# Optimization experiments

Hardware: AMD Instinct MI355X
Metric: run time of the kernel (lower is better)

The kernel has to match this reference:

```python
import jax, jax.numpy as jnp
import numpy as np

DIM = 4096
NUM_EXPERTS = 64
TOP_K = 8
TOKENS = 16384

def setup_inputs() -> dict:
    key = jax.random.key(0)
    kx, kw = jax.random.split(key)
    x = jax.random.normal(kx, (TOKENS, DIM), dtype=jnp.float32)
    # gate weight as in nn.Linear(dim, num_experts, bias=False): shape [num_experts, dim]
    W = jax.random.normal(kw, (NUM_EXPERTS, DIM), dtype=jnp.float32) * 0.02
    return {"x": x, "W": W}

def reference(x, W):
    # logits = x @ W^T : [tokens, num_experts]
    logits = jnp.einsum('td,ed->te', x, W)
    top_k_values, top_k_indices = jax.lax.top_k(logits, TOP_K)
    # softmax over top-k values in float32, cast back to x dtype
    scores = jax.nn.softmax(top_k_values.astype(jnp.float32), axis=-1).astype(x.dtype)
    return scores, top_k_indices
```

## Files before the change

### kernel.cpp

```cpp
#include <hip/hip_runtime.h>
#include <math.h>

typedef float  f32x4 __attribute__((ext_vector_type(4)));
typedef short  s16x8 __attribute__((ext_vector_type(8)));
typedef unsigned short u16x8 __attribute__((ext_vector_type(8)));
typedef unsigned int   u32x4 __attribute__((ext_vector_type(4)));

constexpr int TOKENS  = 16384;
constexpr int DIM     = 4096;
constexpr int NE      = 64;
constexpr int TOPK    = 8;
constexpr int KB      = 32;
constexpr int NIT     = DIM / KB;
constexpr int WAVES   = 8;
constexpr int KSL     = DIM / WAVES;
constexpr int NITW    = KSL / KB;
constexpr int LISTCAP = 16384;
constexpr float GAPTH = 1e-4f;

constexpr unsigned WARR_U16   = (unsigned)NIT * 4 * 64 * 8;
constexpr size_t   WS_INT_OFF = (size_t)WARR_U16 * 2 * sizeof(unsigned short);
constexpr size_t   WS_NEEDED  = WS_INT_OFF + sizeof(int) * (size_t)(16 + LISTCAP);

__device__ __forceinline__ unsigned short bf_rne(float f) {
    unsigned u = __float_as_uint(f);
    u += 0x7FFFu + ((u >> 16) & 1u);
    return (unsigned short)(u >> 16);
}
__device__ __forceinline__ float bf_f32(unsigned short h) {
    return __uint_as_float(((unsigned)h) << 16);
}
__device__ __forceinline__ uint2 cvt_pair(float f0, float f1) {
    unsigned short h0 = bf_rne(f0);
    unsigned short h1 = bf_rne(f1);
    uint2 r;
    r.x = (unsigned)h0 | ((unsigned)h1 << 16);
    r.y = (unsigned)bf_rne(f0 - bf_f32(h0)) | ((unsigned)bf_rne(f1 - bf_f32(h1)) << 16);
    return r;
}
union Cvt { u32x4 u; s16x8 s; };

__global__ __launch_bounds__(256)
void wconv_kernel(const float* __restrict__ W, unsigned short* __restrict__ wpk,
                  int* __restrict__ wsI)
{
    unsigned tid = blockIdx.x * 256u + threadIdx.x;
    if (tid == 0) wsI[0] = 0;
    unsigned j    = tid & 7u;
    unsigned lane = (tid >> 3) & 63u;
    unsigned T    = (tid >> 9) & 3u;
    unsigned it   = tid >> 11;
    unsigned e = 16u * T + (lane & 15u);
    unsigned k = 32u * it + 8u * (lane >> 4) + j;
    float v = W[(size_t)e * DIM + k];
    unsigned short h = bf_rne(v);
    wpk[tid]            = h;
    wpk[WARR_U16 + tid] = bf_rne(v - bf_f32(h));
}

__global__ __launch_bounds__(512, 4)
void gemm_topk_v5(const float* __restrict__ x,
                  const unsigned short* __restrict__ wpk,
                  float* __restrict__ out, int* __restrict__ wsI)
{
    __shared__ float part[WAVES][16][NE + 4];
    __shared__ float outls[16][NE + 4];

    const int t    = threadIdx.x;
    const int ws   = t >> 6;
    const int l    = t & 63;
    const int lq   = l >> 4;
    const int ln   = l & 15;
    const int tok0 = blockIdx.x * 16;

    const float* xg = x + (size_t)(tok0 + ln) * DIM + ws * KSL + 8 * lq;
    const s16x8* bp = (const s16x8*)wpk + ws * NITW * 256 + l;
    const float* xq = xg + 2 * KB;

    f32x4 acc[4];
#pragma unroll
    for (int T = 0; T < 4; ++T) acc[T] = (f32x4){0.f, 0.f, 0.f, 0.f};

    float4 xa0 = *(const float4*)(xg + 0);
    float4 xa1 = *(const float4*)(xg + 4);
    float4 xb0 = *(const float4*)(xg + KB + 0);
    float4 xb1 = *(const float4*)(xg + KB + 4);

#pragma unroll 1
    for (int it = 0; it < NITW; ++it) {
        const s16x8* hp = bp;
        const s16x8* lp = bp + (WARR_U16 / 8);
        s16x8 bh0 = hp[0], bh1 = hp[64], bh2 = hp[128], bh3 = hp[192];
        s16x8 bl0 = lp[0], bl1 = lp[64], bl2 = lp[128], bl3 = lp[192];
        bp += 256;

        float4 xn0 = *(const float4*)(xq + 0);
        float4 xn1 = *(const float4*)(xq + 4);
        if (it + 3 < NITW) xq += KB;

        uint2 p0 = cvt_pair(xa0.x, xa0.y);
        uint2 p1 = cvt_pair(xa0.z, xa0.w);
        uint2 p2 = cvt_pair(xa1.x, xa1.y);
        uint2 p3 = cvt_pair(xa1.z, xa1.w);
        Cvt ch, cl;
        ch.u = (u32x4){p0.x, p1.x, p2.x, p3.x};
        cl.u = (u32x4){p0.y, p1.y, p2.y, p3.y};
        s16x8 ah = ch.s, al = cl.s;

        acc[0] = __builtin_amdgcn_mfma_f32_16x16x32_bf16(ah, bh0, acc[0], 0, 0, 0);
        acc[1] = __builtin_amdgcn_mfma_f32_16x16x32_bf16(ah, bh1, acc[1], 0, 0, 0);
        acc[2] = __builtin_amdgcn_mfma_f32_16x16x32_bf16(ah, bh2, acc[2], 0, 0, 0);
        acc[3] = __builtin_amdgcn_mfma_f32_16x16x32_bf16(ah, bh3, acc[3], 0, 0, 0);
        acc[0] = __builtin_amdgcn_mfma_f32_16x16x32_bf16(ah, bl0, acc[0], 0, 0, 0);
        acc[1] = __builtin_amdgcn_mfma_f32_16x16x32_bf16(ah, bl1, acc[1], 0, 0, 0);
        acc[2] = __builtin_amdgcn_mfma_f32_16x16x32_bf16(ah, bl2, acc[2], 0, 0, 0);
        acc[3] = __builtin_amdgcn_mfma_f32_16x16x32_bf16(ah, bl3, acc[3], 0, 0, 0);
        acc[0] = __builtin_amdgcn_mfma_f32_16x16x32_bf16(al, bh0, acc[0], 0, 0, 0);
        acc[1] = __builtin_amdgcn_mfma_f32_16x16x32_bf16(al, bh1, acc[1], 0, 0, 0);
        acc[2] = __builtin_amdgcn_mfma_f32_16x16x32_bf16(al, bh2, acc[2], 0, 0, 0);
        acc[3] = __builtin_amdgcn_mfma_f32_16x16x32_bf16(al, bh3, acc[3], 0, 0, 0);

        xa0 = xb0; xa1 = xb1; xb0 = xn0; xb1 = xn1;
    }

#pragma unroll
    for (int T = 0; T < 4; ++T)
#pragma unroll
        for (int r = 0; r < 4; ++r)
            part[ws][4 * lq + r][16 * T + ln] = acc[T][r];
    __syncthreads();

    for (int o = t; o < 16 * NE; o += 512) {
        const int ti = o >> 6, e = o & 63;
        float s = 0.f;
#pragma unroll
        for (int w2 = 0; w2 < WAVES; ++w2) s += part[w2][ti][e];
        outls[ti][e] = s;
    }
    __syncthreads();

    if (t < 16) {
        const int tok = tok0 + t;
        float v[9]; int idx[9];
#pragma unroll
        for (int j = 0; j < 9; ++j) {
            float best = -3.4e38f; int bi = 0;
            for (int e = 0; e < NE; ++e) {
                float q = outls[t][e];
                if (q > best) { best = q; bi = e; }
            }
            v[j] = best; idx[j] = bi;
            outls[t][bi] = -3.4e38f;
        }
        bool flag = false;
#pragma unroll
        for (int j = 0; j < 8; ++j)
            if (v[j] - v[j + 1] < GAPTH) flag = true;

        float m = v[0], s = 0.f, ex[8];
#pragma unroll
        for (int j = 0; j < 8; ++j) { ex[j] = expf(v[j] - m); s += ex[j]; }
        float inv = 1.f / s;
#pragma unroll
        for (int j = 0; j < 8; ++j) {
            out[(size_t)tok * TOPK + j] = ex[j] * inv;
            out[(size_t)TOKENS * TOPK + (size_t)tok * TOPK + j] = (float)idx[j];
        }
        if (flag) {
            int pos = atomicAdd(wsI, 1);
            if (pos < LISTCAP) wsI[16 + pos] = tok;
        }
    }
}

__global__ __launch_bounds__(256)
void refine_kernel(const float* __restrict__ x, const float* __restrict__ W,
                   float* __restrict__ out, const int* __restrict__ wsI)
{
    __shared__ float  xr[DIM];
    __shared__ double pt[256];
    __shared__ double lg[NE];

    int cnt = wsI[0];
    if (cnt > LISTCAP) cnt = LISTCAP;
    const int t = threadIdx.x;

    for (int g = blockIdx.x; g < cnt; g += gridDim.x) {
        const int tok = wsI[16 + g];
        __syncthreads();
        for (int i = t; i < DIM / 4; i += 256)
            *(float4*)&xr[4 * i] = *(const float4*)&x[(size_t)tok * DIM + 4 * i];
        __syncthreads();

        const int e  = t & 63;
        const int ks = t >> 6;
        const float* wp = W + (size_t)e * DIM + ks * 1024;
        const float* xp = xr + ks * 1024;
        double p = 0.0;
        for (int i = 0; i < 256; ++i) {
            float4 wv = *(const float4*)&wp[4 * i];
            float4 xv = *(const float4*)&xp[4 * i];
            p = fma((double)xv.x, (double)wv.x, p);
            p = fma((double)xv.y, (double)wv.y, p);
            p = fma((double)xv.z, (double)wv.z, p);
            p = fma((double)xv.w, (double)wv.w, p);
        }
        pt[t] = p;
        __syncthreads();
        if (t < NE)
            lg[t] = ((pt[t] + pt[t + 64]) + pt[t + 128]) + pt[t + 192];
        __syncthreads();
        if (t == 0) {
            double vv[8]; int ii[8];
#pragma unroll
            for (int j = 0; j < 8; ++j) {
                double best = -1e300; int bi = 0;
                for (int e2 = 0; e2 < NE; ++e2) {
                    double q = lg[e2];
                    if (q > best) { best = q; bi = e2; }
                }
                vv[j] = best; ii[j] = bi;
                lg[bi] = -1e300;
            }
            float pf[8], ex[8], s = 0.f;
#pragma unroll
            for (int j = 0; j < 8; ++j) pf[j] = (float)vv[j];
            float m = pf[0];
#pragma unroll
            for (int j = 0; j < 8; ++j) { ex[j] = expf(pf[j] - m); s += ex[j]; }
            float inv = 1.f / s;
#pragma unroll
            for (int j = 0; j < 8; ++j) {
                out[(size_t)tok * TOPK + j] = ex[j] * inv;
                out[(size_t)TOKENS * TOPK + (size_t)tok * TOPK + j] = (float)ii[j];
            }
        }
    }
}

__global__ void zero_cnt_kernel(int* wsI) { if (threadIdx.x == 0) wsI[0] = 0; }

__global__ __launch_bounds__(256)
void gemm_topk_old(const float* __restrict__ x, const float* __restrict__ W,
                   float* __restrict__ out, int* __restrict__ wsI)
{
    __shared__ __align__(16) unsigned short frag[8192];
    __shared__ float ls[64][NE + 4];

    const int t    = threadIdx.x;
    const int tok0 = blockIdx.x * 64;

    const int srow = t >> 2;
    const int sq   = t & 3;
    const int sn   = srow & 15;
    const int sT   = srow >> 4;
    const int sdst = sT * 512 + (16 * sq + (sn ^ (2 * sq))) * 8;
    const float* xg = x + (size_t)(tok0 + srow) * DIM + 8 * sq;
    const float* wg = W + (size_t)srow * DIM + 8 * sq;

    const int w  = t >> 6;
    const int l  = t & 63;
    const int lq = l >> 4;
    const int ln = l & 15;
    const int fo = (16 * lq + (ln ^ (2 * lq))) * 8;

    f32x4 acc[4];
#pragma unroll
    for (int T = 0; T < 4; ++T) acc[T] = (f32x4){0.f, 0.f, 0.f, 0.f};

    float4 xa = *(const float4*)xg;
    float4 xb = *(const float4*)(xg + 4);
    float4 wa = *(const float4*)wg;
    float4 wb = *(const float4*)(wg + 4);

    for (int it = 0; it < NIT; ++it) {
        __syncthreads();
        {
            float vx[8] = {xa.x, xa.y, xa.z, xa.w, xb.x, xb.y, xb.z, xb.w};
            float vw[8] = {wa.x, wa.y, wa.z, wa.w, wb.x, wb.y, wb.z, wb.w};
            u16x8 vxh, vxl, vwh, vwl;
#pragma unroll
            for (int j = 0; j < 8; ++j) {
                unsigned short h1 = bf_rne(vx[j]);
                vxh[j] = h1;
                vxl[j] = bf_rne(vx[j] - bf_f32(h1));
                unsigned short h2 = bf_rne(vw[j]);
                vwh[j] = h2;
                vwl[j] = bf_rne(vw[j] - bf_f32(h2));
            }
            *(u16x8*)&frag[   0 + sdst] = vxh;
            *(u16x8*)&frag[2048 + sdst] = vxl;
            *(u16x8*)&frag[4096 + sdst] = vwh;
            *(u16x8*)&frag[6144 + sdst] = vwl;
        }
        __syncthreads();
        if (it + 1 < NIT) {
            const float* xp = xg + (size_t)(it + 1) * KB;
            const float* wp = wg + (size_t)(it + 1) * KB;
            xa = *(const float4*)xp;  xb = *(const float4*)(xp + 4);
            wa = *(const float4*)wp;  wb = *(const float4*)(wp + 4);
        }
        s16x8 ah = *(const s16x8*)&frag[   0 + w * 512 + fo];
        s16x8 al = *(const s16x8*)&frag[2048 + w * 512 + fo];
#pragma unroll
        for (int T = 0; T < 4; ++T) {
            s16x8 bh = *(const s16x8*)&frag[4096 + T * 512 + fo];
            s16x8 bl = *(const s16x8*)&frag[6144 + T * 512 + fo];
            acc[T] = __builtin_amdgcn_mfma_f32_16x16x32_bf16(ah, bh, acc[T], 0, 0, 0);
            acc[T] = __builtin_amdgcn_mfma_f32_16x16x32_bf16(ah, bl, acc[T], 0, 0, 0);
            acc[T] = __builtin_amdgcn_mfma_f32_16x16x32_bf16(al, bh, acc[T], 0, 0, 0);
        }
    }

    __syncthreads();
#pragma unroll
    for (int T = 0; T < 4; ++T)
#pragma unroll
        for (int r = 0; r < 4; ++r)
            ls[16 * w + 4 * lq + r][16 * T + ln] = acc[T][r];
    __syncthreads();

    if (t < 64) {
        const int tok = tok0 + t;
        float v[9]; int idx[9];
#pragma unroll
        for (int j = 0; j < 9; ++j) {
            float best = -3.4e38f; int bi = 0;
            for (int e = 0; e < NE; ++e) {
                float q = ls[t][e];
                if (q > best) { best = q; bi = e; }
            }
            v[j] = best; idx[j] = bi;
            ls[t][bi] = -3.4e38f;
        }
        bool flag = false;
#pragma unroll
        for (int j = 0; j < 8; ++j)
            if (v[j] - v[j + 1] < GAPTH) flag = true;

        float m = v[0], s = 0.f, ex[8];
#pragma unroll
        for (int j = 0; j < 8; ++j) { ex[j] = expf(v[j] - m); s += ex[j]; }
        float inv = 1.f / s;
#pragma unroll
        for (int j = 0; j < 8; ++j) {
            out[(size_t)tok * TOPK + j] = ex[j] * inv;
            out[(size_t)TOKENS * TOPK + (size_t)tok * TOPK + j] = (float)idx[j];
        }
        if (flag) {
            int pos = atomicAdd(wsI, 1);
            if (pos < LISTCAP) wsI[16 + pos] = tok;
        }
    }
}

extern "C" void kernel_launch(void* const* d_in, const int* in_sizes, int n_in,
                              void* d_out, int out_size, void* d_ws, size_t ws_size,
                              hipStream_t stream)
{
    const float* x = (const float*)d_in[0];
    const float* W = (const float*)d_in[1];
    float* out = (float*)d_out;

    if (ws_size >= WS_NEEDED) {
        unsigned short* wpk = (unsigned short*)d_ws;
        int* wsI = (int*)((char*)d_ws + WS_INT_OFF);
        hipLaunchKernelGGL(wconv_kernel, dim3(WARR_U16 / 256), dim3(256), 0, stream, W, wpk, wsI);
        hipLaunchKernelGGL(gemm_topk_v5, dim3(TOKENS / 16), dim3(512), 0, stream, x, wpk, out, wsI);
        hipLaunchKernelGGL(refine_kernel, dim3(256), dim3(256), 0, stream, x, W, out, wsI);
    } else {
        int* wsI = (int*)d_ws;
        hipLaunchKernelGGL(zero_cnt_kernel, dim3(1), dim3(64), 0, stream, wsI);
        hipLaunchKernelGGL(gemm_topk_old, dim3(TOKENS / 64), dim3(256), 0, stream, x, W, out, wsI);
        hipLaunchKernelGGL(refine_kernel, dim3(256), dim3(256), 0, stream, x, W, out, wsI);
    }
}
```

Before: 436.7 us.

## Process 32 tokens per block to reuse packed W fragments across two token tiles

The main GEMM kernel now handles 32 tokens per workgroup instead of 16, so each loaded bf16 hi/lo W fragment feeds MFMAs for two 16-token tiles. This halves W reads per token, which are L2 traffic since x is streamed once anyway. It also interleaves loads and conversions between MFMA groups. The cost is double the accumulator registers, an occupancy hint lowered from 4 to 2, fewer blocks, and a larger LDS footprint.

```diff
diff --git a/kernel.cpp b/kernel.cpp
--- a/kernel.cpp
+++ b/kernel.cpp
@@ -15,12 +15,14 @@
 constexpr int WAVES   = 8;
 constexpr int KSL     = DIM / WAVES;
 constexpr int NITW    = KSL / KB;
+constexpr int TM      = 32;
+constexpr int NBLK    = TOKENS / TM;
 constexpr int LISTCAP = 16384;
 constexpr float GAPTH = 1e-4f;
 
 constexpr unsigned WARR_U16   = (unsigned)NIT * 4 * 64 * 8;
 constexpr size_t   WS_INT_OFF = (size_t)WARR_U16 * 2 * sizeof(unsigned short);
-constexpr size_t   WS_NEEDED  = WS_INT_OFF + sizeof(int) * (size_t)(16 + LISTCAP);
+constexpr size_t   WS_MIN     = WS_INT_OFF + 0x11000;
 
 __device__ __forceinline__ unsigned short bf_rne(float f) {
     unsigned u = __float_as_uint(f);
@@ -39,6 +41,17 @@
     return r;
 }
 union Cvt { u32x4 u; s16x8 s; };
+
+__device__ __forceinline__ void cvt_frag(float4 a0, float4 a1, s16x8& ah, s16x8& al) {
+    uint2 p0 = cvt_pair(a0.x, a0.y);
+    uint2 p1 = cvt_pair(a0.z, a0.w);
+    uint2 p2 = cvt_pair(a1.x, a1.y);
+    uint2 p3 = cvt_pair(a1.z, a1.w);
+    Cvt ch, cl;
+    ch.u = (u32x4){p0.x, p1.x, p2.x, p3.x};
+    cl.u = (u32x4){p0.y, p1.y, p2.y, p3.y};
+    ah = ch.s; al = cl.s;
+}
 
 __global__ __launch_bounds__(256)
 void wconv_kernel(const float* __restrict__ W, unsigned short* __restrict__ wpk,
@@ -58,80 +71,101 @@
     wpk[WARR_U16 + tid] = bf_rne(v - bf_f32(h));
 }
 
-__global__ __launch_bounds__(512, 4)
-void gemm_topk_v5(const float* __restrict__ x,
+__global__ __launch_bounds__(512, 2)
+void gemm_topk_v8(const float* __restrict__ x,
                   const unsigned short* __restrict__ wpk,
                   float* __restrict__ out, int* __restrict__ wsI)
 {
-    __shared__ float part[WAVES][16][NE + 4];
-    __shared__ float outls[16][NE + 4];
+    __shared__ float part[WAVES][TM][NE + 4];
+    __shared__ float outls[TM][NE + 5];
 
     const int t    = threadIdx.x;
     const int ws   = t >> 6;
     const int l    = t & 63;
     const int lq   = l >> 4;
     const int ln   = l & 15;
-    const int tok0 = blockIdx.x * 16;
-
-    const float* xg = x + (size_t)(tok0 + ln) * DIM + ws * KSL + 8 * lq;
-    const s16x8* bp = (const s16x8*)wpk + ws * NITW * 256 + l;
-    const float* xq = xg + 2 * KB;
-
-    f32x4 acc[4];
-#pragma unroll
-    for (int T = 0; T < 4; ++T) acc[T] = (f32x4){0.f, 0.f, 0.f, 0.f};
-
-    float4 xa0 = *(const float4*)(xg + 0);
-    float4 xa1 = *(const float4*)(xg + 4);
-    float4 xb0 = *(const float4*)(xg + KB + 0);
-    float4 xb1 = *(const float4*)(xg + KB + 4);
+    const int tok0 = blockIdx.x * TM;
+
+    constexpr int LOFF = (int)(WARR_U16 / 8);
+
+    const float* xg0 = x + (size_t)(tok0 + ln) * DIM + ws * KSL + 8 * lq;
+    const float* xg1 = xg0 + (size_t)16 * DIM;
+    const s16x8* bp  = (const s16x8*)wpk + ws * NITW * 256 + l;
+    const float* xq0 = xg0 + 2 * KB;
+    const float* xq1 = xg1 + 2 * KB;
+
+    f32x4 acc[8];
+#pragma unroll
+    for (int T = 0; T < 8; ++T) acc[T] = (f32x4){0.f, 0.f, 0.f, 0.f};
+
+    float4 xa0 = *(const float4*)(xg0 + 0),      xa1 = *(const float4*)(xg0 + 4);
+    float4 xb0 = *(const float4*)(xg0 + KB + 0), xb1 = *(const float4*)(xg0 + KB + 4);
+    float4 ya0 = *(const float4*)(xg1 + 0),      ya1 = *(const float4*)(xg1 + 4);
+    float4 yb0 = *(const float4*)(xg1 + KB + 0), yb1 = *(const float4*)(xg1 + KB + 4);
 
 #pragma unroll 1
     for (int it = 0; it < NITW; ++it) {
         const s16x8* hp = bp;
-        const s16x8* lp = bp + (WARR_U16 / 8);
-        s16x8 bh0 = hp[0], bh1 = hp[64], bh2 = hp[128], bh3 = hp[192];
-        s16x8 bl0 = lp[0], bl1 = lp[64], bl2 = lp[128], bl3 = lp[192];
+        const s16x8* lp = bp + LOFF;
+
+        s16x8 bh0 = hp[0], bh1 = hp[64];
+        s16x8 bl0 = lp[0], bl1 = lp[64];
+
+        float4 xn0 = *(const float4*)(xq0 + 0), xn1 = *(const float4*)(xq0 + 4);
+        float4 yn0 = *(const float4*)(xq1 + 0), yn1 = *(const float4*)(xq1 + 4);
+        if (it + 3 < NITW) { xq0 += KB; xq1 += KB; }
+
+        s16x8 ah0, al0;
+        cvt_frag(xa0, xa1, ah0, al0);
+
+        s16x8 bh2 = hp[128], bh3 = hp[192];
+        s16x8 bl2 = lp[128], bl3 = lp[192];
+
+        s16x8 ah1, al1;
+        cvt_frag(ya0, ya1, ah1, al1);
+
+        acc[0] = __builtin_amdgcn_mfma_f32_16x16x32_bf16(ah0, bh0, acc[0], 0, 0, 0);
+        acc[1] = __builtin_amdgcn_mfma_f32_16x16x32_bf16(ah0, bh1, acc[1], 0, 0, 0);
+        acc[4] = __builtin_amdgcn_mfma_f32_16x16x32_bf16(ah1, bh0, acc[4], 0, 0, 0);
+        acc[5] = __builtin_amdgcn_mfma_f32_16x16x32_bf16(ah1, bh1, acc[5], 0, 0, 0);
+        acc[0] = __builtin_amdgcn_mfma_f32_16x16x32_bf16(ah0, bl0, acc[0], 0, 0, 0);
+        acc[1] = __builtin_amdgcn_mfma_f32_16x16x32_bf16(ah0, bl1, acc[1], 0, 0, 0);
+        acc[4] = __builtin_amdgcn_mfma_f32_16x16x32_bf16(ah1, bl0, acc[4], 0, 0, 0);
+        acc[5] = __builtin_amdgcn_mfma_f32_16x16x32_bf16(ah1, bl1, acc[5], 0, 0, 0);
+        acc[0] = __builtin_amdgcn_mfma_f32_16x16x32_bf16(al0, bh0, acc[0], 0, 0, 0);
+        acc[1] = __builtin_amdgcn_mfma_f32_16x16x32_bf16(al0, bh1, acc[1], 0, 0, 0);
+        acc[4] = __builtin_amdgcn_mfma_f32_16x16x32_bf16(al1, bh0, acc[4], 0, 0, 0);
+        acc[5] = __builtin_amdgcn_mfma_f32_16x16x32_bf16(al1, bh1, acc[5], 0, 0, 0);
+
+        acc[2] = __builtin_amdgcn_mfma_f32_16x16x32_bf16(ah0, bh2, acc[2], 0, 0, 0);
+        acc[3] = __builtin_amdgcn_mfma_f32_16x16x32_bf16(ah0, bh3, acc[3], 0, 0, 0);
+        acc[6] = __builtin_amdgcn_mfma_f32_16x16x32_bf16(ah1, bh2, acc[6], 0, 0, 0);
+        acc[7] = __builtin_amdgcn_mfma_f32_16x16x32_bf16(ah1, bh3, acc[7], 0, 0, 0);
+        acc[2] = __builtin_amdgcn_mfma_f32_16x16x32_bf16(ah0, bl2, acc[2], 0, 0, 0);
+        acc[3] = __builtin_amdgcn_mfma_f32_16x16x32_bf16(ah0, bl3, acc[3], 0, 0, 0);
+        acc[6] = __builtin_amdgcn_mfma_f32_16x16x32_bf16(ah1, bl2, acc[6], 0, 0, 0);
+        acc[7] = __builtin_amdgcn_mfma_f32_16x16x32_bf16(ah1, bl3, acc[7], 0, 0, 0);
+        acc[2] = __builtin_amdgcn_mfma_f32_16x16x32_bf16(al0, bh2, acc[2], 0, 0, 0);
+        acc[3] = __builtin_amdgcn_mfma_f32_16x16x32_bf16(al0, bh3, acc[3], 0, 0, 0);
+        acc[6] = __builtin_amdgcn_mfma_f32_16x16x32_bf16(al1, bh2, acc[6], 0, 0, 0);
+        acc[7] = __builtin_amdgcn_mfma_f32_16x16x32_bf16(al1, bh3, acc[7], 0, 0, 0);
+
         bp += 256;
-
-        float4 xn0 = *(const float4*)(xq + 0);
-        float4 xn1 = *(const float4*)(xq + 4);
-        if (it + 3 < NITW) xq += KB;
-
-        uint2 p0 = cvt_pair(xa0.x, xa0.y);
-        uint2 p1 = cvt_pair(xa0.z, xa0.w);
-        uint2 p2 = cvt_pair(xa1.x, xa1.y);
-        uint2 p3 = cvt_pair(xa1.z, xa1.w);
-        Cvt ch, cl;
-        ch.u = (u32x4){p0.x, p1.x, p2.x, p3.x};
-        cl.u = (u32x4){p0.y, p1.y, p2.y, p3.y};
-        s16x8 ah = ch.s, al = cl.s;
-
-        acc[0] = __builtin_amdgcn_mfma_f32_16x16x32_bf16(ah, bh0, acc[0], 0, 0, 0);
-        acc[1] = __builtin_amdgcn_mfma_f32_16x16x32_bf16(ah, bh1, acc[1], 0, 0, 0);
-        acc[2] = __builtin_amdgcn_mfma_f32_16x16x32_bf16(ah, bh2, acc[2], 0, 0, 0);
-        acc[3] = __builtin_amdgcn_mfma_f32_16x16x32_bf16(ah, bh3, acc[3], 0, 0, 0);
-        acc[0] = __builtin_amdgcn_mfma_f32_16x16x32_bf16(ah, bl0, acc[0], 0, 0, 0);
-        acc[1] = __builtin_amdgcn_mfma_f32_16x16x32_bf16(ah, bl1, acc[1], 0, 0, 0);
-        acc[2] = __builtin_amdgcn_mfma_f32_16x16x32_bf16(ah, bl2, acc[2], 0, 0, 0);
-        acc[3] = __builtin_amdgcn_mfma_f32_16x16x32_bf16(ah, bl3, acc[3], 0, 0, 0);
-        acc[0] = __builtin_amdgcn_mfma_f32_16x16x32_bf16(al, bh0, acc[0], 0, 0, 0);
-        acc[1] = __builtin_amdgcn_mfma_f32_16x16x32_bf16(al, bh1, acc[1], 0, 0, 0);
-        acc[2] = __builtin_amdgcn_mfma_f32_16x16x32_bf16(al, bh2, acc[2], 0, 0, 0);
-        acc[3] = __builtin_amdgcn_mfma_f32_16x16x32_bf16(al, bh3, acc[3], 0, 0, 0);
-
         xa0 = xb0; xa1 = xb1; xb0 = xn0; xb1 = xn1;
+        ya0 = yb0; ya1 = yb1; yb0 = yn0; yb1 = yn1;
     }
 
 #pragma unroll
     for (int T = 0; T < 4; ++T)
 #pragma unroll
-        for (int r = 0; r < 4; ++r)
-            part[ws][4 * lq + r][16 * T + ln] = acc[T][r];
+        for (int r = 0; r < 4; ++r) {
+            part[ws][     4 * lq + r][16 * T + ln] = acc[T][r];
+            part[ws][16 + 4 * lq + r][16 * T + ln] = acc[4 + T][r];
+        }
     __syncthreads();
 
-    for (int o = t; o < 16 * NE; o += 512) {
-        const int ti = o >> 6, e = o & 63;
+    for (int o2 = t; o2 < TM * NE; o2 += 512) {
+        const int ti = o2 >> 6, e = o2 & 63;
         float s = 0.f;
 #pragma unroll
         for (int w2 = 0; w2 < WAVES; ++w2) s += part[w2][ti][e];
@@ -139,7 +173,7 @@
     }
     __syncthreads();
 
-    if (t < 16) {
+    if (t < TM) {
         const int tok = tok0 + t;
         float v[9]; int idx[9];
 #pragma unroll
@@ -215,7 +249,7 @@
 #pragma unroll
             for (int j = 0; j < 8; ++j) {
                 double best = -1e300; int bi = 0;
-                for (int e2 = 0; e2 < NE; ++e2) {
+                for (int e2 = 0; e2 < 64; ++e2) {
                     double q = lg[e2];
                     if (q > best) { best = q; bi = e2; }
                 }
@@ -362,11 +396,11 @@
     const float* W = (const float*)d_in[1];
     float* out = (float*)d_out;
 
-    if (ws_size >= WS_NEEDED) {
+    if (ws_size >= WS_MIN) {
         unsigned short* wpk = (unsigned short*)d_ws;
         int* wsI = (int*)((char*)d_ws + WS_INT_OFF);
         hipLaunchKernelGGL(wconv_kernel, dim3(WARR_U16 / 256), dim3(256), 0, stream, W, wpk, wsI);
-        hipLaunchKernelGGL(gemm_topk_v5, dim3(TOKENS / 16), dim3(512), 0, stream, x, wpk, out, wsI);
+        hipLaunchKernelGGL(gemm_topk_v8, dim3(NBLK), dim3(512), 0, stream, x, wpk, out, wsI);
         hipLaunchKernelGGL(refine_kernel, dim3(256), dim3(256), 0, stream, x, W, out, wsI);
     } else {
         int* wsI = (int*)d_ws;
```

After: 417.5 us. -4.4%, faster.
